# Kernel optimization log

Measured on AMD Instinct MI355X. Metric: run time of the kernel, lower is better.

Reference implementation:

```python
import jax, jax.numpy as jnp
import numpy as np

S = 7          # grid side
B = 2          # boxes per cell
C = 20         # classes
COORD = 5.0    # coord_scale
NOOBJ = 0.5    # noobj_scale
CELL = B * 5 + C


def _corners(box):
    # box [..., >=4] with (x_cell, y_cell, w, h); convert to (x1,y1,x2,y2)
    s = 1.0 / S
    xy = box[..., :2] * s
    wh = box[..., 2:4]
    return jnp.concatenate([xy - 0.5 * wh, xy + 0.5 * wh], axis=-1)


def setup_inputs() -> dict:
    key = jax.random.key(0)
    k1, k2, k3 = jax.random.split(key, 3)
    preds = jax.random.uniform(k1, (16384, S, S, CELL), dtype=jnp.float32)
    labels = jax.random.uniform(k2, (16384, S, S, CELL), dtype=jnp.float32)
    conf = labels[..., 4]
    conf = jnp.where(conf > 0.8, conf, 0.0)
    labels = labels.at[..., 4].set(conf)
    return {"preds": preds, "labels": labels}


def reference(preds, labels):
    N = preds.shape[0]
    p = preds.reshape(-1, CELL)   # [M, 30]
    l = labels.reshape(-1, CELL)
    obj = l[:, 4] > 0             # [M] object cells
    noobj = ~obj

    conf_idx = jnp.arange(B) * 5 + 4  # confidence channel per box

    # --- noobj confidence loss (only confidence channels of noobj cells) ---
    d_noobj = p[:, conf_idx] - l[:, conf_idx]           # [M, B]
    noobj_loss = jnp.sum(jnp.where(noobj[:, None], d_noobj * d_noobj, 0.0))

    # --- per-cell box tensors ---
    bp = p[:, :B * 5].reshape(-1, B, 5)  # [M, B, 5] predicted boxes
    bl = l[:, :B * 5].reshape(-1, B, 5)  # [M, B, 5] label boxes

    # IoU of each predicted box vs the cell's ground-truth box (label box 0).
    # Torch builds fresh FloatTensors for the corner coords and uses
    # max_iou.data, so no gradient flows through the matching -> stop_gradient.
    pc = _corners(bp)            # [M, B, 4]
    gt = _corners(bl[:, 0, :])   # [M, 4]
    ix1 = jnp.maximum(pc[..., 0], gt[:, None, 0])
    iy1 = jnp.maximum(pc[..., 1], gt[:, None, 1])
    ix2 = jnp.minimum(pc[..., 2], gt[:, None, 2])
    iy2 = jnp.minimum(pc[..., 3], gt[:, None, 3])
    inter = jnp.clip(ix2 - ix1, 0.0) * jnp.clip(iy2 - iy1, 0.0)
    a1 = (pc[..., 2] - pc[..., 0]) * (pc[..., 3] - pc[..., 1])
    a2 = (gt[:, 2] - gt[:, 0]) * (gt[:, 3] - gt[:, 1])
    iou = jax.lax.stop_gradient(inter / (a1 + a2[:, None] - inter))  # [M, B]

    best = jnp.argmax(iou, axis=1)          # [M]
    max_iou = jnp.max(iou, axis=1)          # [M]
    resp = jax.nn.one_hot(best, B, dtype=jnp.bool_)  # [M, B]
    resp_mask = resp & obj[:, None]                   # responsible boxes
    notresp_mask = (~resp) & obj[:, None]             # other boxes in obj cells

    # --- coord losses on responsible boxes ---
    d_xy = bp[..., :2] - bl[..., :2]
    xy_loss = jnp.sum(jnp.where(resp_mask[..., None], d_xy * d_xy, 0.0))
    d_wh = jnp.sqrt(bp[..., 2:4]) - jnp.sqrt(bl[..., 2:4])
    wh_loss = jnp.sum(jnp.where(resp_mask[..., None], d_wh * d_wh, 0.0))

    # --- confidence losses ---
    d_resp = bp[..., 4] - max_iou[:, None]  # target conf = matched IoU
    response_loss = jnp.sum(jnp.where(resp_mask, d_resp * d_resp, 0.0))
    not_response_loss = jnp.sum(jnp.where(notresp_mask, bp[..., 4] ** 2, 0.0))

    # --- class loss on obj cells ---
    d_cls = p[:, B * 5:] - l[:, B * 5:]
    class_loss = jnp.sum(jnp.where(obj[:, None], d_cls * d_cls, 0.0))

    total = (COORD * (xy_loss + wh_loss) + 2.0 * response_loss
             + not_response_loss + NOOBJ * noobj_loss + class_loss)
    return total / N
```

## Files before the change

kernel.cpp:

```cpp
#include <hip/hip_runtime.h>

namespace {

constexpr int NCLS   = 20;
constexpr int NIMG   = 16384;
constexpr int NCELLS = NIMG * 7 * 7;
constexpr int BLOCK  = 256;
constexpr int NBLK   = NCELLS / 2 / BLOCK;

__device__ __forceinline__ float cell_loss(const float* __restrict__ p,
                                           const float* __restrict__ l) {
  const float l4 = l[4];
  if (!(l4 > 0.0f)) {
    float d4 = p[4] - l4;
    float d9 = p[9] - l[9];
    return 0.5f * (d4 * d4 + d9 * d9);
  }
  const float sc = 1.0f / 7.0f;
  float gcx = l[0] * sc, gcy = l[1] * sc, gw = l[2], gh = l[3];
  float gx1 = gcx - 0.5f * gw, gy1 = gcy - 0.5f * gh;
  float gx2 = gcx + 0.5f * gw, gy2 = gcy + 0.5f * gh;
  float a2 = (gx2 - gx1) * (gy2 - gy1);

  float iou0 = 0.0f, iou1 = 0.0f;
#pragma unroll
  for (int b = 0; b < 2; ++b) {
    const float* bp = p + 5 * b;
    float cx = bp[0] * sc, cy = bp[1] * sc, w = bp[2], h = bp[3];
    float x1 = cx - 0.5f * w, y1 = cy - 0.5f * h;
    float x2 = cx + 0.5f * w, y2 = cy + 0.5f * h;
    float ix1 = fmaxf(x1, gx1), iy1 = fmaxf(y1, gy1);
    float ix2 = fminf(x2, gx2), iy2 = fminf(y2, gy2);
    float inter = fmaxf(ix2 - ix1, 0.0f) * fmaxf(iy2 - iy1, 0.0f);
    float a1 = (x2 - x1) * (y2 - y1);
    float v = inter / (a1 + a2 - inter);
    if (b == 0) iou0 = v; else iou1 = v;
  }
  int r = (iou1 > iou0) ? 1 : 0;
  float miou = fmaxf(iou0, iou1);
  const float* rp = p + 5 * r;
  const float* rl = l + 5 * r;

  float dx = rp[0] - rl[0], dy = rp[1] - rl[1];
  float xy = dx * dx + dy * dy;
  float dw = sqrtf(rp[2]) - sqrtf(rl[2]);
  float dh = sqrtf(rp[3]) - sqrtf(rl[3]);
  float wh = dw * dw + dh * dh;
  float dr = rp[4] - miou;
  float nr = p[5 * (1 - r) + 4];
  float cls = 0.0f;
#pragma unroll
  for (int c = 0; c < NCLS; ++c) {
    float d = p[10 + c] - l[10 + c];
    cls = fmaf(d, d, cls);
  }
  return 5.0f * (xy + wh) + 2.0f * (dr * dr) + nr * nr + cls;
}

__global__ __launch_bounds__(BLOCK) void yolo_loss_main(
    const float* __restrict__ preds, const float* __restrict__ labels,
    double* __restrict__ acc) {
  __shared__ float wsum[BLOCK / 64];

  const int t = threadIdx.x;
  const long long g = (long long)blockIdx.x * BLOCK + t;
  const float4* gp4 = reinterpret_cast<const float4*>(preds) + g * 15;
  const float4* gl4 = reinterpret_cast<const float4*>(labels) + g * 15;

  float p[60], l[60];
#pragma unroll
  for (int k = 0; k < 15; ++k) {
    float4 vp = gp4[k];
    float4 vl = gl4[k];
    p[4 * k] = vp.x; p[4 * k + 1] = vp.y; p[4 * k + 2] = vp.z; p[4 * k + 3] = vp.w;
    l[4 * k] = vl.x; l[4 * k + 1] = vl.y; l[4 * k + 2] = vl.z; l[4 * k + 3] = vl.w;
  }

  float v = cell_loss(p, l) + cell_loss(p + 30, l + 30);

#pragma unroll
  for (int off = 32; off > 0; off >>= 1) v += __shfl_down(v, off);
  if ((t & 63) == 0) wsum[t >> 6] = v;
  __syncthreads();
  if (t == 0) {
    float bs = (wsum[0] + wsum[1]) + (wsum[2] + wsum[3]);
    atomicAdd(acc, (double)bs);
  }
}

__global__ void yolo_loss_finalize(const double* __restrict__ acc,
                                   float* __restrict__ out) {
  out[0] = (float)(acc[0] * (1.0 / (double)NIMG));
}

}

extern "C" void kernel_launch(void* const* d_in, const int* in_sizes, int n_in,
                              void* d_out, int out_size, void* d_ws, size_t ws_size,
                              hipStream_t stream) {
  const float* preds  = (const float*)d_in[0];
  const float* labels = (const float*)d_in[1];
  double* acc = (double*)d_ws;
  hipMemsetAsync(d_ws, 0, sizeof(double), stream);
  yolo_loss_main<<<NBLK, BLOCK, 0, stream>>>(preds, labels, acc);
  yolo_loss_finalize<<<1, 1, 0, stream>>>(acc, (float*)d_out);
}
```

Before: 46.94 us.

## Stage cell tiles through LDS with coalesced loads in a persistent grid

Each thread used to read its two cells directly from global memory as strided float4 loads of 240 bytes per thread. Now a 64-thread block stages a 64-cell tile of preds and labels into shared memory with fully coalesced float4 loads, then each thread computes one cell's loss from LDS. A grid-stride persistent loop over tiles also cuts the block count and the number of atomics. The cost is two barriers per tile and a loop with no software prefetch, which may expose load latency, and only one wave per block.

```diff
diff --git a/kernel.cpp b/kernel.cpp
--- a/kernel.cpp
+++ b/kernel.cpp
@@ -5,8 +5,9 @@
 constexpr int NCLS   = 20;
 constexpr int NIMG   = 16384;
 constexpr int NCELLS = NIMG * 7 * 7;
-constexpr int BLOCK  = 256;
-constexpr int NBLK   = NCELLS / 2 / BLOCK;
+constexpr int TILE   = 64;
+constexpr int NT     = NCELLS / TILE;
+constexpr int NB     = 2560;
 
 __device__ __forceinline__ float cell_loss(const float* __restrict__ p,
                                            const float* __restrict__ l) {
@@ -57,35 +58,32 @@
   return 5.0f * (xy + wh) + 2.0f * (dr * dr) + nr * nr + cls;
 }
 
-__global__ __launch_bounds__(BLOCK) void yolo_loss_main(
+__global__ __launch_bounds__(64) void yolo_loss_main(
     const float* __restrict__ preds, const float* __restrict__ labels,
     double* __restrict__ acc) {
-  __shared__ float wsum[BLOCK / 64];
+  __shared__ float4 s[960];
 
-  const int t = threadIdx.x;
-  const long long g = (long long)blockIdx.x * BLOCK + t;
-  const float4* gp4 = reinterpret_cast<const float4*>(preds) + g * 15;
-  const float4* gl4 = reinterpret_cast<const float4*>(labels) + g * 15;
+  const int lane = threadIdx.x;
+  float vsum = 0.0f;
 
-  float p[60], l[60];
+  for (int tile = blockIdx.x; tile < NT; tile += NB) {
+    const float4* pb = reinterpret_cast<const float4*>(preds) + (size_t)tile * 480;
+    const float4* lb = reinterpret_cast<const float4*>(labels) + (size_t)tile * 480;
 #pragma unroll
-  for (int k = 0; k < 15; ++k) {
-    float4 vp = gp4[k];
-    float4 vl = gl4[k];
-    p[4 * k] = vp.x; p[4 * k + 1] = vp.y; p[4 * k + 2] = vp.z; p[4 * k + 3] = vp.w;
-    l[4 * k] = vl.x; l[4 * k + 1] = vl.y; l[4 * k + 2] = vl.z; l[4 * k + 3] = vl.w;
+    for (int k = 0; k < 15; ++k) {
+      int r = k * 64 + lane;
+      s[r] = (r < 480) ? pb[r] : lb[r - 480];
+    }
+    __syncthreads();
+    const float* p = reinterpret_cast<const float*>(s) + lane * 30;
+    const float* l = reinterpret_cast<const float*>(s) + 1920 + lane * 30;
+    vsum += cell_loss(p, l);
+    __syncthreads();
   }
 
-  float v = cell_loss(p, l) + cell_loss(p + 30, l + 30);
-
 #pragma unroll
-  for (int off = 32; off > 0; off >>= 1) v += __shfl_down(v, off);
-  if ((t & 63) == 0) wsum[t >> 6] = v;
-  __syncthreads();
-  if (t == 0) {
-    float bs = (wsum[0] + wsum[1]) + (wsum[2] + wsum[3]);
-    atomicAdd(acc, (double)bs);
-  }
+  for (int off = 32; off > 0; off >>= 1) vsum += __shfl_down(vsum, off);
+  if (lane == 0) atomicAdd(acc, (double)vsum);
 }
 
 __global__ void yolo_loss_finalize(const double* __restrict__ acc,
@@ -102,6 +100,6 @@
   const float* labels = (const float*)d_in[1];
   double* acc = (double*)d_ws;
   hipMemsetAsync(d_ws, 0, sizeof(double), stream);
-  yolo_loss_main<<<NBLK, BLOCK, 0, stream>>>(preds, labels, acc);
+  yolo_loss_main<<<NB, TILE, 0, stream>>>(preds, labels, acc);
   yolo_loss_finalize<<<1, 1, 0, stream>>>(acc, (float*)d_out);
 }
```

After: 61.95 us. 32.0% more time.
